# Kernel tuning notes

Hardware: AMD Instinct MI355X
Metric: run time of the kernel (lower is better)

The kernel has to match this reference:

```python
import jax, jax.numpy as jnp
import numpy as np

N, E = 50000, 800000
IN_DIM, HID, H, L = 256, 128, 4, 2
HD = HID // H
EPS = 1e-5


def _bn(x, g, b):
    # training-mode BatchNorm1d: biased variance over batch dim, eps=1e-5
    m = x.mean(0)
    v = jnp.var(x, axis=0)
    return g * (x - m) * jax.lax.rsqrt(v + EPS) + b


def _seg_softmax(scores, dst, n):
    # scores: [E, H]; softmax over edges sharing the same dst node
    m = jax.ops.segment_max(scores, dst, num_segments=n)  # [N, H]
    e = jnp.exp(scores - m[dst])
    s = jax.ops.segment_sum(e, dst, num_segments=n)
    return e / s[dst]


def _attn_layer(h, src, dst, wq, bq, wk, bk, wv, bv, wo, bo):
    n = h.shape[0]
    scale = 1.0 / np.sqrt(HD)
    Q = (h @ wq + bq).reshape(n, H, HD)
    K = (h @ wk + bk).reshape(n, H, HD)
    V = (h @ wv + bv).reshape(n, H, HD)
    # per-edge scores: Q of src dotted with K of dst
    scores = jnp.einsum('ehd,ehd->eh', Q[src], K[dst]) * scale  # [E, H]
    attn = _seg_softmax(scores, dst, n)                         # [E, H]
    # weighted scatter-sum of V gathered at dst (faithful to source)
    out = jax.ops.segment_sum(attn[:, :, None] * V[dst], dst, num_segments=n)
    out = out.reshape(n, HID) @ wo + bo
    return jax.nn.relu(out)


def setup_inputs() -> dict:
    key = jax.random.key(0)
    ks = jax.random.split(key, 20)
    s = 0.05  # weight scale to keep activations tame
    inp = {
        'x': jax.random.normal(ks[0], (N, IN_DIM), jnp.float32),
        'edge_index': jax.random.randint(ks[1], (2, E), 0, N),
        'W_enc1': jax.random.normal(ks[2], (IN_DIM, HID), jnp.float32) * s,
        'b_enc1': jax.random.normal(ks[3], (HID,), jnp.float32) * s,
        'g1': jnp.ones((HID,), jnp.float32),
        'beta1': jnp.zeros((HID,), jnp.float32),
        'W_enc2': jax.random.normal(ks[4], (HID, HID), jnp.float32) * s,
        'b_enc2': jax.random.normal(ks[5], (HID,), jnp.float32) * s,
        'g2': jnp.ones((HID,), jnp.float32),
        'beta2': jnp.zeros((HID,), jnp.float32),
        'Wq': jax.random.normal(ks[6], (L, HID, HID), jnp.float32) * s,
        'bq': jax.random.normal(ks[7], (L, HID), jnp.float32) * s,
        'Wk': jax.random.normal(ks[8], (L, HID, HID), jnp.float32) * s,
        'bk': jax.random.normal(ks[9], (L, HID), jnp.float32) * s,
        'Wv': jax.random.normal(ks[10], (L, HID, HID), jnp.float32) * s,
        'bv': jax.random.normal(ks[11], (L, HID), jnp.float32) * s,
        'Wo': jax.random.normal(ks[12], (L, HID, HID), jnp.float32) * s,
        'bo': jax.random.normal(ks[13], (L, HID), jnp.float32) * s,
    }
    return inp


def reference(x, edge_index, W_enc1, b_enc1, g1, beta1, W_enc2, b_enc2, g2, beta2,
              Wq, bq, Wk, bk, Wv, bv, Wo, bo):
    src, dst = edge_index[0], edge_index[1]
    # encoder: Linear -> BN -> ReLU -> (dropout=id) -> Linear -> BN -> ReLU
    h = jax.nn.relu(_bn(x @ W_enc1 + b_enc1, g1, beta1))
    h = jax.nn.relu(_bn(h @ W_enc2 + b_enc2, g2, beta2))
    for i in range(L):
        h = _attn_layer(h, src, dst, Wq[i], bq[i], Wk[i], bk[i],
                        Wv[i], bv[i], Wo[i], bo[i])
    return h
```

## Files before the change

kernel.cpp:

```cpp
#include <hip/hip_runtime.h>

#define NN 50000
#define NE 800000
#define NB 1563
#define TOTF 114688

typedef unsigned short u16;
typedef unsigned int u32;
typedef __attribute__((ext_vector_type(8))) short s8v;
typedef __attribute__((ext_vector_type(4))) float f4v;

__device__ __forceinline__ void split2(float f, u16& h, u16& lo) {
    u32 u = __float_as_uint(f);
    h = (u16)(u >> 16);
    float r = f - __uint_as_float(u & 0xFFFF0000u);
    lo = (u16)(__float_as_uint(r) >> 16);
}

__global__ void prep_k(float* __restrict__ mask,
                       const float* __restrict__ W1, const float* __restrict__ W2,
                       const float* __restrict__ Wv, const float* __restrict__ Wo,
                       u16* __restrict__ fh, u16* __restrict__ fl) {
    int i = blockIdx.x * 256 + threadIdx.x;
    if (i < NN) mask[i] = 0.f;
    if (i < TOTF) {
        const float* W;
        int local;
        if (i < 32768) { W = W1; local = i; }
        else {
            int t = i - 32768;
            int m = t >> 14;
            local = t & 16383;
            if (m == 0) W = W2;
            else if (m == 1) W = Wv;
            else if (m == 2) W = Wo;
            else if (m == 3) W = Wv + 16384;
            else W = Wo + 16384;
        }
        int j = local & 7, l = (local >> 3) & 63, nt = (local >> 9) & 7, kc = local >> 12;
        int k = kc * 32 + ((l >> 4) << 3) + j;
        int n = nt * 16 + (l & 15);
        u16 h, lo;
        split2(W[k * 128 + n], h, lo);
        fh[i] = h;
        fl[i] = lo;
    }
}

__global__ __launch_bounds__(64)
void redstats_k(const float* __restrict__ pst, float* __restrict__ st) {
    int c = blockIdx.x;
    float s = 0.f;
    for (int b = threadIdx.x; b < NB; b += 64) s += pst[(size_t)c * NB + b];
    s += __shfl_xor(s, 1);  s += __shfl_xor(s, 2);  s += __shfl_xor(s, 4);
    s += __shfl_xor(s, 8);  s += __shfl_xor(s, 16); s += __shfl_xor(s, 32);
    if (threadIdx.x == 0) st[c] = s;
}

template<int KC, int FOLD, int STATS, int SCAT>
__global__ __launch_bounds__(128, 4)
void mgemm_k(const float* __restrict__ A,
             const u16* __restrict__ fh, const u16* __restrict__ fl,
             const float* __restrict__ bias,
             const float* __restrict__ fst,
             const float* __restrict__ fg, const float* __restrict__ fbe,
             const int* __restrict__ dstv,
             float* __restrict__ maskw,
             float* __restrict__ pst,
             float* __restrict__ C) {
    constexpr int KP = KC / 4;
    __shared__ __align__(16) u16 Ah[2][16][136];
    __shared__ __align__(16) u16 Al[2][16][136];
    const int tid = threadIdx.x;
    const int l = tid & 63, w = tid >> 6;
    const int q = l >> 4, cc = l & 15;
    const int wrow0 = blockIdx.x * 32 + w * 16;
    const int c0 = (l & 31) * 4;

    if (SCAT) {
        for (int e = blockIdx.x * 128 + tid; e < NE; e += NB * 128)
            maskw[dstv[e]] = 1.0f;
    }

    float ga[4], sh[4];
    if (FOLD) {
#pragma unroll
        for (int m = 0; m < 4; ++m) {
            int c = c0 + m;
            float mean = fst[c] * (1.0f / NN);
            float var = fst[128 + c] * (1.0f / NN) - mean * mean;
            float gi = fg[c] * rsqrtf(var + 1e-5f);
            ga[m] = gi;
            sh[m] = fbe[c] - mean * gi;
        }
    }

    f4v zf = {0.f, 0.f, 0.f, 0.f};
    f4v acc[8];
#pragma unroll
    for (int t = 0; t < 8; ++t) acc[t] = zf;

    for (int p = 0; p < KP; ++p) {
#pragma unroll
        for (int it = 0; it < 8; ++it) {
            int r = (l >> 5) + 2 * it;
            int gr = wrow0 + r; if (gr > NN - 1) gr = NN - 1;
            float4 f = *(const float4*)(A + (size_t)gr * (KC * 32) + p * 128 + c0);
            float v[4] = {f.x, f.y, f.z, f.w};
            if (FOLD) {
#pragma unroll
                for (int m = 0; m < 4; ++m) {
                    float t = v[m] * ga[m] + sh[m];
                    v[m] = t > 0.f ? t : 0.f;
                }
            }
            ushort4 uh, ul;
            split2(v[0], uh.x, ul.x); split2(v[1], uh.y, ul.y);
            split2(v[2], uh.z, ul.z); split2(v[3], uh.w, ul.w);
            *(ushort4*)&Ah[w][r][c0] = uh;
            *(ushort4*)&Al[w][r][c0] = ul;
        }
#pragma unroll
        for (int kc = 0; kc < 4; ++kc) {
            int kcg = p * 4 + kc;
            s8v ah = *(const s8v*)&Ah[w][cc][kc * 32 + q * 8];
            s8v al = *(const s8v*)&Al[w][cc][kc * 32 + q * 8];
#pragma unroll
            for (int t = 0; t < 8; ++t) {
                const int fo = kcg * 4096 + t * 512 + l * 8;
                s8v bh = *(const s8v*)(fh + fo);
                s8v bl = *(const s8v*)(fl + fo);
                acc[t] = __builtin_amdgcn_mfma_f32_16x16x32_bf16(ah, bh, acc[t], 0, 0, 0);
                acc[t] = __builtin_amdgcn_mfma_f32_16x16x32_bf16(ah, bl, acc[t], 0, 0, 0);
                acc[t] = __builtin_amdgcn_mfma_f32_16x16x32_bf16(al, bh, acc[t], 0, 0, 0);
            }
        }
    }

    float ps[8], pq[8];
#pragma unroll
    for (int t = 0; t < 8; ++t) { ps[t] = 0.f; pq[t] = 0.f; }
#pragma unroll
    for (int t = 0; t < 8; ++t) {
        int col = t * 16 + cc;
        float bb = bias[col];
#pragma unroll
        for (int r = 0; r < 4; ++r) {
            int gr = wrow0 + q * 4 + r;
            float val = acc[t][r] + bb;
            if (gr < NN) {
                C[(size_t)gr * 128 + col] = val;
                if (STATS) { ps[t] += val; pq[t] += val * val; }
            }
        }
    }
    if (STATS) {
#pragma unroll
        for (int t = 0; t < 8; ++t) {
            ps[t] += __shfl_xor(ps[t], 16); ps[t] += __shfl_xor(ps[t], 32);
            pq[t] += __shfl_xor(pq[t], 16); pq[t] += __shfl_xor(pq[t], 32);
        }
        __syncthreads();
        float* wr = (float*)&Ah[0][0][0];
        if (l < 16) {
#pragma unroll
            for (int t = 0; t < 8; ++t) {
                int col = t * 16 + l;
                wr[w * 256 + col] = ps[t];
                wr[w * 256 + 128 + col] = pq[t];
            }
        }
        __syncthreads();
        {
            int c = tid;
            pst[(size_t)c * NB + blockIdx.x]         = wr[c] + wr[256 + c];
            pst[(size_t)(128 + c) * NB + blockIdx.x] = wr[128 + c] + wr[384 + c];
        }
    }
}

__global__ __launch_bounds__(128, 4)
void mmega_k(const float* __restrict__ X,
             const u16* __restrict__ fh, const u16* __restrict__ fl,
             const float* __restrict__ bv, const float* __restrict__ bo,
             const float* __restrict__ fst,
             const float* __restrict__ fg, const float* __restrict__ fbe,
             const float* __restrict__ mask, float* __restrict__ out) {
    __shared__ __align__(16) u16 Ah[2][16][136];
    __shared__ __align__(16) u16 Al[2][16][136];
    const int tid = threadIdx.x;
    const int l = tid & 63, w = tid >> 6;
    const int q = l >> 4, cc = l & 15;
    const int wrow0 = blockIdx.x * 32 + w * 16;
    const int c0 = (l & 31) * 4;

    float ga[4], sh[4];
#pragma unroll
    for (int m = 0; m < 4; ++m) {
        int c = c0 + m;
        float mean = fst[c] * (1.0f / NN);
        float var = fst[128 + c] * (1.0f / NN) - mean * mean;
        float gi = fg[c] * rsqrtf(var + 1e-5f);
        ga[m] = gi;
        sh[m] = fbe[c] - mean * gi;
    }

    float rm[4];
#pragma unroll
    for (int r = 0; r < 4; ++r) {
        int gr = wrow0 + q * 4 + r;
        rm[r] = (gr < NN) ? mask[gr] : 0.f;
    }

#pragma unroll
    for (int it = 0; it < 8; ++it) {
        int r = (l >> 5) + 2 * it;
        int gr = wrow0 + r; if (gr > NN - 1) gr = NN - 1;
        float4 f = *(const float4*)(X + (size_t)gr * 128 + c0);
        float v[4] = {f.x, f.y, f.z, f.w};
#pragma unroll
        for (int m = 0; m < 4; ++m) {
            float t = v[m] * ga[m] + sh[m];
            v[m] = t > 0.f ? t : 0.f;
        }
        ushort4 uh, ul;
        split2(v[0], uh.x, ul.x); split2(v[1], uh.y, ul.y);
        split2(v[2], uh.z, ul.z); split2(v[3], uh.w, ul.w);
        *(ushort4*)&Ah[w][r][c0] = uh;
        *(ushort4*)&Al[w][r][c0] = ul;
    }

    f4v zf = {0.f, 0.f, 0.f, 0.f};
    for (int s = 0; s < 4; ++s) {
        const u16* WH = fh + s * 16384;
        const u16* WL = fl + s * 16384;
        const float* bp = (s == 0) ? bv : (s == 1) ? bo : (s == 2) ? (bv + 128) : (bo + 128);

        f4v acc[8];
#pragma unroll
        for (int t = 0; t < 8; ++t) acc[t] = zf;
#pragma unroll
        for (int kc = 0; kc < 4; ++kc) {
            s8v ah = *(const s8v*)&Ah[w][cc][kc * 32 + q * 8];
            s8v al = *(const s8v*)&Al[w][cc][kc * 32 + q * 8];
#pragma unroll
            for (int t = 0; t < 8; ++t) {
                const int fo = kc * 4096 + t * 512 + l * 8;
                s8v bh = *(const s8v*)(WH + fo);
                s8v bl = *(const s8v*)(WL + fo);
                acc[t] = __builtin_amdgcn_mfma_f32_16x16x32_bf16(ah, bh, acc[t], 0, 0, 0);
                acc[t] = __builtin_amdgcn_mfma_f32_16x16x32_bf16(ah, bl, acc[t], 0, 0, 0);
                acc[t] = __builtin_amdgcn_mfma_f32_16x16x32_bf16(al, bh, acc[t], 0, 0, 0);
            }
        }

        if (s == 3) {
#pragma unroll
            for (int t = 0; t < 8; ++t) {
                int col = t * 16 + cc;
                float bb = bp[col];
#pragma unroll
                for (int r = 0; r < 4; ++r) {
                    int gr = wrow0 + q * 4 + r;
                    if (gr < NN)
                        out[(size_t)gr * 128 + col] = fmaxf(acc[t][r] + bb, 0.f);
                }
            }
        } else {
#pragma unroll
            for (int t = 0; t < 8; ++t) {
                int col = t * 16 + cc;
                float bb = bp[col];
#pragma unroll
                for (int r = 0; r < 4; ++r) {
                    int rl = q * 4 + r;
                    float val = acc[t][r] + bb;
                    val = (s == 1) ? fmaxf(val, 0.f) : val * rm[r];
                    u16 h, lo; split2(val, h, lo);
                    Ah[w][rl][col] = h;
                    Al[w][rl][col] = lo;
                }
            }
        }
    }
}

extern "C" void kernel_launch(void* const* d_in, const int* in_sizes, int n_in,
                              void* d_out, int out_size, void* d_ws, size_t ws_size,
                              hipStream_t stream) {
    const float* x   = (const float*)d_in[0];
    const int*   ei  = (const int*)d_in[1];
    const float* W1  = (const float*)d_in[2];
    const float* b1  = (const float*)d_in[3];
    const float* g1  = (const float*)d_in[4];
    const float* be1 = (const float*)d_in[5];
    const float* W2  = (const float*)d_in[6];
    const float* b2  = (const float*)d_in[7];
    const float* g2  = (const float*)d_in[8];
    const float* be2 = (const float*)d_in[9];
    const float* Wv  = (const float*)d_in[14];
    const float* bv  = (const float*)d_in[15];
    const float* Wo  = (const float*)d_in[16];
    const float* bo  = (const float*)d_in[17];

    float* out = (float*)d_out;

    char* ws = (char*)d_ws;
    float* buf  = (float*)(ws);
    float* mask = (float*)(ws + 25600000);
    float* st1  = (float*)(ws + 25800704);
    float* st2  = st1 + 256;
    u16*   fH   = (u16*)(ws + 25804800);
    u16*   fL   = fH + TOTF;
    float* pst  = (float*)(ws + 26263552);

    prep_k<<<dim3((TOTF + 255) / 256), dim3(256), 0, stream>>>(
        mask, W1, W2, Wv, Wo, fH, fL);

    dim3 gg(NB), bb(128);
    mgemm_k<8, 0, 1, 1><<<gg, bb, 0, stream>>>(x, fH, fL, b1,
                                               nullptr, nullptr, nullptr,
                                               ei + NE, mask, pst, buf);
    redstats_k<<<dim3(256), dim3(64), 0, stream>>>(pst, st1);
    mgemm_k<4, 1, 1, 0><<<gg, bb, 0, stream>>>(buf, fH + 32768, fL + 32768, b2,
                                               st1, g1, be1,
                                               nullptr, nullptr, pst, out);
    redstats_k<<<dim3(256), dim3(64), 0, stream>>>(pst, st2);
    mmega_k<<<gg, bb, 0, stream>>>(out, fH + 49152, fL + 49152, bv, bo,
                                   st2, g2, be2, mask, out);
}
```

Baseline: 234.6 us.

## Split GEMM tiles across warps by column, prefetch A, transpose partial-stats layout

The two waves in a block now share one 32-row LDS tile and each computes half of the output columns for both 16-row slices. Before, each wave owned 16 rows and loaded all 128 columns of weight fragments, so this halves per-wave weight fragment loads. The A tile is register-prefetched one K-panel ahead with nontemporal loads, and outputs use nontemporal stores. Partial BN statistics are written block-major so stores coalesce, and the reduction kernel reads them strided to match. The cost is extra __syncthreads barriers, since the LDS tile is now shared between waves.

Result: no change. 233.9 us (-0.3%).

```diff
diff --git a/kernel.cpp b/kernel.cpp
--- a/kernel.cpp
+++ b/kernel.cpp
@@ -9,6 +9,7 @@
 typedef unsigned int u32;
 typedef __attribute__((ext_vector_type(8))) short s8v;
 typedef __attribute__((ext_vector_type(4))) float f4v;
+typedef __attribute__((ext_vector_type(4))) float nf4;
 
 __device__ __forceinline__ void split2(float f, u16& h, u16& lo) {
     u32 u = __float_as_uint(f);
@@ -51,7 +52,7 @@
 void redstats_k(const float* __restrict__ pst, float* __restrict__ st) {
     int c = blockIdx.x;
     float s = 0.f;
-    for (int b = threadIdx.x; b < NB; b += 64) s += pst[(size_t)c * NB + b];
+    for (int b = threadIdx.x; b < NB; b += 64) s += pst[(size_t)b * 256 + c];
     s += __shfl_xor(s, 1);  s += __shfl_xor(s, 2);  s += __shfl_xor(s, 4);
     s += __shfl_xor(s, 8);  s += __shfl_xor(s, 16); s += __shfl_xor(s, 32);
     if (threadIdx.x == 0) st[c] = s;
@@ -69,13 +70,14 @@
              float* __restrict__ pst,
              float* __restrict__ C) {
     constexpr int KP = KC / 4;
-    __shared__ __align__(16) u16 Ah[2][16][136];
-    __shared__ __align__(16) u16 Al[2][16][136];
+    __shared__ __align__(16) u16 Ah[32][136];
+    __shared__ __align__(16) u16 Al[32][136];
     const int tid = threadIdx.x;
     const int l = tid & 63, w = tid >> 6;
     const int q = l >> 4, cc = l & 15;
-    const int wrow0 = blockIdx.x * 32 + w * 16;
-    const int c0 = (l & 31) * 4;
+    const int row0 = blockIdx.x * 32;
+    const int c0 = (tid & 31) * 4;
+    const int r0 = tid >> 5;
 
     if (SCAT) {
         for (int e = blockIdx.x * 128 + tid; e < NE; e += NB * 128)
@@ -96,17 +98,26 @@
     }
 
     f4v zf = {0.f, 0.f, 0.f, 0.f};
-    f4v acc[8];
-#pragma unroll
-    for (int t = 0; t < 8; ++t) acc[t] = zf;
+    f4v acc[2][4];
+#pragma unroll
+    for (int s = 0; s < 2; ++s)
+#pragma unroll
+        for (int t = 0; t < 4; ++t) acc[s][t] = zf;
+
+    nf4 pref[8];
+#pragma unroll
+    for (int it = 0; it < 8; ++it) {
+        int gr = row0 + r0 + 4 * it; if (gr > NN - 1) gr = NN - 1;
+        pref[it] = __builtin_nontemporal_load(
+            (const nf4*)(A + (size_t)gr * (KC * 32) + c0));
+    }
 
     for (int p = 0; p < KP; ++p) {
+        if (p > 0) __syncthreads();
 #pragma unroll
         for (int it = 0; it < 8; ++it) {
-            int r = (l >> 5) + 2 * it;
-            int gr = wrow0 + r; if (gr > NN - 1) gr = NN - 1;
-            float4 f = *(const float4*)(A + (size_t)gr * (KC * 32) + p * 128 + c0);
-            float v[4] = {f.x, f.y, f.z, f.w};
+            int r = r0 + 4 * it;
+            float v[4] = {pref[it].x, pref[it].y, pref[it].z, pref[it].w};
             if (FOLD) {
 #pragma unroll
                 for (int m = 0; m < 4; ++m) {
@@ -117,64 +128,73 @@
             ushort4 uh, ul;
             split2(v[0], uh.x, ul.x); split2(v[1], uh.y, ul.y);
             split2(v[2], uh.z, ul.z); split2(v[3], uh.w, ul.w);
-            *(ushort4*)&Ah[w][r][c0] = uh;
-            *(ushort4*)&Al[w][r][c0] = ul;
+            *(ushort4*)&Ah[r][c0] = uh;
+            *(ushort4*)&Al[r][c0] = ul;
+        }
+        __syncthreads();
+        if (p + 1 < KP) {
+#pragma unroll
+            for (int it = 0; it < 8; ++it) {
+                int gr = row0 + r0 + 4 * it; if (gr > NN - 1) gr = NN - 1;
+                pref[it] = __builtin_nontemporal_load(
+                    (const nf4*)(A + (size_t)gr * (KC * 32) + (p + 1) * 128 + c0));
+            }
         }
 #pragma unroll
         for (int kc = 0; kc < 4; ++kc) {
             int kcg = p * 4 + kc;
-            s8v ah = *(const s8v*)&Ah[w][cc][kc * 32 + q * 8];
-            s8v al = *(const s8v*)&Al[w][cc][kc * 32 + q * 8];
-#pragma unroll
-            for (int t = 0; t < 8; ++t) {
-                const int fo = kcg * 4096 + t * 512 + l * 8;
+            s8v ah0 = *(const s8v*)&Ah[cc][kc * 32 + q * 8];
+            s8v al0 = *(const s8v*)&Al[cc][kc * 32 + q * 8];
+            s8v ah1 = *(const s8v*)&Ah[16 + cc][kc * 32 + q * 8];
+            s8v al1 = *(const s8v*)&Al[16 + cc][kc * 32 + q * 8];
+#pragma unroll
+            for (int t = 0; t < 4; ++t) {
+                const int fo = kcg * 4096 + (4 * w + t) * 512 + l * 8;
                 s8v bh = *(const s8v*)(fh + fo);
                 s8v bl = *(const s8v*)(fl + fo);
-                acc[t] = __builtin_amdgcn_mfma_f32_16x16x32_bf16(ah, bh, acc[t], 0, 0, 0);
-                acc[t] = __builtin_amdgcn_mfma_f32_16x16x32_bf16(ah, bl, acc[t], 0, 0, 0);
-                acc[t] = __builtin_amdgcn_mfma_f32_16x16x32_bf16(al, bh, acc[t], 0, 0, 0);
-            }
-        }
-    }
-
-    float ps[8], pq[8];
-#pragma unroll
-    for (int t = 0; t < 8; ++t) { ps[t] = 0.f; pq[t] = 0.f; }
-#pragma unroll
-    for (int t = 0; t < 8; ++t) {
-        int col = t * 16 + cc;
+                acc[0][t] = __builtin_amdgcn_mfma_f32_16x16x32_bf16(ah0, bh, acc[0][t], 0, 0, 0);
+                acc[0][t] = __builtin_amdgcn_mfma_f32_16x16x32_bf16(ah0, bl, acc[0][t], 0, 0, 0);
+                acc[0][t] = __builtin_amdgcn_mfma_f32_16x16x32_bf16(al0, bh, acc[0][t], 0, 0, 0);
+                acc[1][t] = __builtin_amdgcn_mfma_f32_16x16x32_bf16(ah1, bh, acc[1][t], 0, 0, 0);
+                acc[1][t] = __builtin_amdgcn_mfma_f32_16x16x32_bf16(ah1, bl, acc[1][t], 0, 0, 0);
+                acc[1][t] = __builtin_amdgcn_mfma_f32_16x16x32_bf16(al1, bh, acc[1][t], 0, 0, 0);
+            }
+        }
+    }
+
+    float ps[4], pq[4];
+#pragma unroll
+    for (int t = 0; t < 4; ++t) { ps[t] = 0.f; pq[t] = 0.f; }
+#pragma unroll
+    for (int t = 0; t < 4; ++t) {
+        int col = (4 * w + t) * 16 + cc;
         float bb = bias[col];
 #pragma unroll
-        for (int r = 0; r < 4; ++r) {
-            int gr = wrow0 + q * 4 + r;
-            float val = acc[t][r] + bb;
-            if (gr < NN) {
-                C[(size_t)gr * 128 + col] = val;
-                if (STATS) { ps[t] += val; pq[t] += val * val; }
+        for (int sl = 0; sl < 2; ++sl) {
+#pragma unroll
+            for (int r = 0; r < 4; ++r) {
+                int gr = row0 + sl * 16 + q * 4 + r;
+                float val = acc[sl][t][r] + bb;
+                if (gr < NN) {
+                    __builtin_nontemporal_store(val, &C[(size_t)gr * 128 + col]);
+                    if (STATS) { ps[t] += val; pq[t] += val * val; }
+                }
             }
         }
     }
     if (STATS) {
 #pragma unroll
-        for (int t = 0; t < 8; ++t) {
+        for (int t = 0; t < 4; ++t) {
             ps[t] += __shfl_xor(ps[t], 16); ps[t] += __shfl_xor(ps[t], 32);
             pq[t] += __shfl_xor(pq[t], 16); pq[t] += __shfl_xor(pq[t], 32);
         }
-        __syncthreads();
-        float* wr = (float*)&Ah[0][0][0];
         if (l < 16) {
 #pragma unroll
-            for (int t = 0; t < 8; ++t) {
-                int col = t * 16 + l;
-                wr[w * 256 + col] = ps[t];
-                wr[w * 256 + 128 + col] = pq[t];
-            }
-        }
-        __syncthreads();
-        {
-            int c = tid;
-            pst[(size_t)c * NB + blockIdx.x]         = wr[c] + wr[256 + c];
-            pst[(size_t)(128 + c) * NB + blockIdx.x] = wr[128 + c] + wr[384 + c];
+            for (int t = 0; t < 4; ++t) {
+                int col = (4 * w + t) * 16 + l;
+                pst[(size_t)blockIdx.x * 256 + col] = ps[t];
+                pst[(size_t)blockIdx.x * 256 + 128 + col] = pq[t];
+            }
         }
     }
 }
@@ -186,13 +206,14 @@
              const float* __restrict__ fst,
              const float* __restrict__ fg, const float* __restrict__ fbe,
              const float* __restrict__ mask, float* __restrict__ out) {
-    __shared__ __align__(16) u16 Ah[2][16][136];
-    __shared__ __align__(16) u16 Al[2][16][136];
+    __shared__ __align__(16) u16 Ah[32][136];
+    __shared__ __align__(16) u16 Al[32][136];
     const int tid = threadIdx.x;
     const int l = tid & 63, w = tid >> 6;
     const int q = l >> 4, cc = l & 15;
-    const int wrow0 = blockIdx.x * 32 + w * 16;
-    const int c0 = (l & 31) * 4;
+    const int row0 = blockIdx.x * 32;
+    const int c0 = (tid & 31) * 4;
+    const int r0 = tid >> 5;
 
     float ga[4], sh[4];
 #pragma unroll
@@ -205,18 +226,21 @@
         sh[m] = fbe[c] - mean * gi;
     }
 
-    float rm[4];
-#pragma unroll
-    for (int r = 0; r < 4; ++r) {
-        int gr = wrow0 + q * 4 + r;
-        rm[r] = (gr < NN) ? mask[gr] : 0.f;
-    }
+    float rm[2][4];
+#pragma unroll
+    for (int sl = 0; sl < 2; ++sl)
+#pragma unroll
+        for (int r = 0; r < 4; ++r) {
+            int gr = row0 + sl * 16 + q * 4 + r;
+            rm[sl][r] = (gr < NN) ? mask[gr] : 0.f;
+        }
 
 #pragma unroll
     for (int it = 0; it < 8; ++it) {
-        int r = (l >> 5) + 2 * it;
-        int gr = wrow0 + r; if (gr > NN - 1) gr = NN - 1;
-        float4 f = *(const float4*)(X + (size_t)gr * 128 + c0);
+        int r = r0 + 4 * it;
+        int gr = row0 + r; if (gr > NN - 1) gr = NN - 1;
+        nf4 f = __builtin_nontemporal_load(
+            (const nf4*)(X + (size_t)gr * 128 + c0));
         float v[4] = {f.x, f.y, f.z, f.w};
 #pragma unroll
         for (int m = 0; m < 4; ++m) {
@@ -226,9 +250,10 @@
         ushort4 uh, ul;
         split2(v[0], uh.x, ul.x); split2(v[1], uh.y, ul.y);
         split2(v[2], uh.z, ul.z); split2(v[3], uh.w, ul.w);
-        *(ushort4*)&Ah[w][r][c0] = uh;
-        *(ushort4*)&Al[w][r][c0] = ul;
-    }
+        *(ushort4*)&Ah[r][c0] = uh;
+        *(ushort4*)&Al[r][c0] = ul;
+    }
+    __syncthreads();
 
     f4v zf = {0.f, 0.f, 0.f, 0.f};
     for (int s = 0; s < 4; ++s) {
@@ -236,51 +261,66 @@
         const u16* WL = fl + s * 16384;
         const float* bp = (s == 0) ? bv : (s == 1) ? bo : (s == 2) ? (bv + 128) : (bo + 128);
 
-        f4v acc[8];
-#pragma unroll
-        for (int t = 0; t < 8; ++t) acc[t] = zf;
+        f4v acc[2][4];
+#pragma unroll
+        for (int sl = 0; sl < 2; ++sl)
+#pragma unroll
+            for (int t = 0; t < 4; ++t) acc[sl][t] = zf;
 #pragma unroll
         for (int kc = 0; kc < 4; ++kc) {
-            s8v ah = *(const s8v*)&Ah[w][cc][kc * 32 + q * 8];
-            s8v al = *(const s8v*)&Al[w][cc][kc * 32 + q * 8];
-#pragma unroll
-            for (int t = 0; t < 8; ++t) {
-                const int fo = kc * 4096 + t * 512 + l * 8;
+            s8v ah0 = *(const s8v*)&Ah[cc][kc * 32 + q * 8];
+            s8v al0 = *(const s8v*)&Al[cc][kc * 32 + q * 8];
+            s8v ah1 = *(const s8v*)&Ah[16 + cc][kc * 32 + q * 8];
+            s8v al1 = *(const s8v*)&Al[16 + cc][kc * 32 + q * 8];
+#pragma unroll
+            for (int t = 0; t < 4; ++t) {
+                const int fo = kc * 4096 + (4 * w + t) * 512 + l * 8;
                 s8v bh = *(const s8v*)(WH + fo);
                 s8v bl = *(const s8v*)(WL + fo);
-                acc[t] = __builtin_amdgcn_mfma_f32_16x16x32_bf16(ah, bh, acc[t], 0, 0, 0);
-                acc[t] = __builtin_amdgcn_mfma_f32_16x16x32_bf16(ah, bl, acc[t], 0, 0, 0);
-                acc[t] = __builtin_amdgcn_mfma_f32_16x16x32_bf16(al, bh, acc[t], 0, 0, 0);
+                acc[0][t] = __builtin_amdgcn_mfma_f32_16x16x32_bf16(ah0, bh, acc[0][t], 0, 0, 0);
+                acc[0][t] = __builtin_amdgcn_mfma_f32_16x16x32_bf16(ah0, bl, acc[0][t], 0, 0, 0);
+                acc[0][t] = __builtin_amdgcn_mfma_f32_16x16x32_bf16(al0, bh, acc[0][t], 0, 0, 0);
+                acc[1][t] = __builtin_amdgcn_mfma_f32_16x16x32_bf16(ah1, bh, acc[1][t], 0, 0, 0);
+                acc[1][t] = __builtin_amdgcn_mfma_f32_16x16x32_bf16(ah1, bl, acc[1][t], 0, 0, 0);
+                acc[1][t] = __builtin_amdgcn_mfma_f32_16x16x32_bf16(al1, bh, acc[1][t], 0, 0, 0);
             }
         }
 
         if (s == 3) {
 #pragma unroll
-            for (int t = 0; t < 8; ++t) {
-                int col = t * 16 + cc;
+            for (int t = 0; t < 4; ++t) {
+                int col = (4 * w + t) * 16 + cc;
                 float bb = bp[col];
 #pragma unroll
-                for (int r = 0; r < 4; ++r) {
-                    int gr = wrow0 + q * 4 + r;
-                    if (gr < NN)
-                        out[(size_t)gr * 128 + col] = fmaxf(acc[t][r] + bb, 0.f);
-                }
+                for (int sl = 0; sl < 2; ++sl)
+#pragma unroll
+                    for (int r = 0; r < 4; ++r) {
+                        int gr = row0 + sl * 16 + q * 4 + r;
+                        if (gr < NN)
+                            __builtin_nontemporal_store(
+                                fmaxf(acc[sl][t][r] + bb, 0.f),
+                                &out[(size_t)gr * 128 + col]);
+                    }
             }
         } else {
-#pragma unroll
-            for (int t = 0; t < 8; ++t) {
-                int col = t * 16 + cc;
+            __syncthreads();
+#pragma unroll
+            for (int t = 0; t < 4; ++t) {
+                int col = (4 * w + t) * 16 + cc;
                 float bb = bp[col];
 #pragma unroll
-                for (int r = 0; r < 4; ++r) {
-                    int rl = q * 4 + r;
-                    float val = acc[t][r] + bb;
-                    val = (s == 1) ? fmaxf(val, 0.f) : val * rm[r];
-                    u16 h, lo; split2(val, h, lo);
-                    Ah[w][rl][col] = h;
-                    Al[w][rl][col] = lo;
-                }
-            }
+                for (int sl = 0; sl < 2; ++sl)
+#pragma unroll
+                    for (int r = 0; r < 4; ++r) {
+                        int rl = sl * 16 + q * 4 + r;
+                        float val = acc[sl][t][r] + bb;
+                        val = (s == 1) ? fmaxf(val, 0.f) : val * rm[sl][r];
+                        u16 h, lo; split2(val, h, lo);
+                        Ah[rl][col] = h;
+                        Al[rl][col] = lo;
+                    }
+            }
+            __syncthreads();
         }
     }
 }
```
